# Performance work log

Measured on AMD Instinct MI355X. Metric: run time of the kernel, lower is better.

The kernel has to match this reference:

```python
import jax, jax.numpy as jnp
import numpy as np

# ---- module configuration (from init_kwargs) ----
NX, NV = 2048, 1024
LX = 1.0
VMAX = 6.0
DX = LX / NX
DV = 2.0 * VMAX / NV
XS = jnp.linspace(-LX / 2 + DX / 2, LX / 2 - DX / 2, NX)
VS = jnp.linspace(-VMAX + DV / 2, VMAX - DV / 2, NV)
AE, AI = 1.0, 1836.0
ZE, ZI = -1.0, 1.0
OMEGA_C_TAU = 1.0
NU_EE, NU_II = 1.0, 0.1
DT = 1e-3
T_LBO = 1.0  # LBO temperature, u = 0


def minmod(a, b):
    return jnp.where(a * b > 0, jnp.sign(a) * jnp.minimum(jnp.abs(a), jnp.abs(b)), 0.0)


def _sl(a, lo, hi, axis):
    return jax.lax.slice_in_dim(a, lo, hi, axis=axis)


def slope_limited_flux_divergence(f_pad, F, dx, axis):
    # f_pad has N+4 cells along `axis` (2 ghost cells per side). MUSCL + minmod.
    n = f_pad.shape[axis]
    d = _sl(f_pad, 1, n, axis) - _sl(f_pad, 0, n - 1, axis)          # n-1 diffs
    sigma = minmod(_sl(d, 0, n - 2, axis), _sl(d, 1, n - 1, axis))    # slopes for cells 1..n-2
    fc = _sl(f_pad, 1, n - 1, axis)                                   # cells 1..n-2
    m = n - 2
    fL = _sl(fc, 0, m - 1, axis) + 0.5 * _sl(sigma, 0, m - 1, axis)   # left interface states
    fR = _sl(fc, 1, m, axis) - 0.5 * _sl(sigma, 1, m, axis)           # right interface states
    flux = F(fL, fR)                                                  # N+1 interface fluxes
    k = flux.shape[axis]
    return (_sl(flux, 1, k, axis) - _sl(flux, 0, k - 1, axis)) / dx   # N cells


def pad_x_periodic(f):
    return jnp.concatenate([f[-2:, :], f, f[:2, :]], axis=0)


def pad_v_zero(f):
    z = jnp.zeros((f.shape[0], 2), f.dtype)
    return jnp.concatenate([z, f, z], axis=1)


def poisson_solve(rho_c):
    # dE/dx = rho_c, zero-mean E (periodic-compatible gauge)
    E = jnp.cumsum(rho_c) * DX
    return E - jnp.mean(E)


def species_rhs(f, E, A, Z):
    v = VS[None, :]
    Fx = lambda l, r: jnp.where(v > 0, l * v, r * v)                  # upwind in x
    vdfdx = slope_limited_flux_divergence(pad_x_periodic(f), Fx, DX, axis=0)
    Ec = (OMEGA_C_TAU * Z / A) * E[:, None]
    Fv = lambda l, r: jnp.where(Ec > 0, l * Ec, r * Ec)               # upwind in v
    Edfdv = slope_limited_flux_divergence(pad_v_zero(f), Fv, DV, axis=1)
    return -vdfdx - Edfdv


def vlasov_rhs(fe, fi):
    ne = jnp.sum(fe, axis=1) * DV
    ni = jnp.sum(fi, axis=1) * DV
    E = poisson_solve(ZE * ne + ZI * ni)
    return species_rhs(fe, E, AE, ZE), species_rhs(fi, E, AI, ZI)


def ssprk2(fe, fi, dt):
    re, ri = vlasov_rhs(fe, fi)
    fe1, fi1 = fe + dt * re, fi + dt * ri
    re1, ri1 = vlasov_rhs(fe1, fi1)
    return 0.5 * (fe + fe1 + dt * re1), 0.5 * (fi + fi1 + dt * ri1)


def lbo_diagonals(lam):
    # L f = lam * d/dv( v f + T df/dv ), central differences
    vm = jnp.roll(VS, 1)
    vp = jnp.roll(VS, -1)
    dl = lam * (T_LBO / DV**2 - vm / (2 * DV))
    du = lam * (T_LBO / DV**2 + vp / (2 * DV))
    d = lam * (-2.0 * T_LBO / DV**2) * jnp.ones(NV, XS.dtype)
    return dl.at[0].set(0.0), d, du.at[-1].set(0.0)


def nu_shape():
    midpt = LX / 3
    ef = LX / 6 / 10
    h0 = lambda x: 1 + jnp.exp(x / ef - midpt / ef)
    return 1.0 / (0.5 * (h0(XS) + h0(-XS)))  # [Nx]


def thomas(dl, d, du, b):
    # Thomas algorithm; dl[0]==0 and du[-1]==0 assumed.
    def fwd(carry, inp):
        cp, bp = carry
        dli, di, dui, bi = inp
        m = di - dli * cp
        cpi = dui / m
        bpi = (bi - dli * bp) / m
        return (cpi, bpi), (cpi, bpi)
    z = jnp.zeros((), b.dtype)
    _, (cp, bp) = jax.lax.scan(fwd, (z, z), (dl, d, du, b))
    def bwd(x_next, inp):
        cpi, bpi = inp
        x = bpi - cpi * x_next
        return x, x
    _, x = jax.lax.scan(bwd, z, (cp, bp), reverse=True)
    return x


def implicit_collide(f, lam, dt):
    dl, d, du = lbo_diagonals(lam)
    nu = nu_shape()
    def solve_row(nui, frow):
        return thomas(-dt * nui * dl, 1.0 - dt * nui * d, -dt * nui * du, frow)
    return jax.vmap(solve_row)(nu, f)


def setup_inputs() -> dict:
    key = jax.random.key(0)
    k1, k2 = jax.random.split(key)
    fe = jax.random.uniform(k1, (NX, NV), dtype=jnp.float32)
    fi = jax.random.uniform(k2, (NX, NV), dtype=jnp.float32)
    return {"fe": fe, "fi": fi}


def reference(fe, fi):
    fe1, fi1 = ssprk2(fe, fi, DT)
    fe2 = implicit_collide(fe1, NU_EE, DT)
    fi2 = implicit_collide(fi1, NU_II, DT)
    return jnp.stack([fe2, fi2])  # [2, Nx, Nv]
```

## Files before the change

kernel.cpp:

```cpp
#include <hip/hip_runtime.h>
#include <math.h>

#define NX 2048
#define NV 1024

static constexpr float DXf    = 1.0f / 2048.0f;
static constexpr float DVf    = 12.0f / 1024.0f;
static constexpr float DTf    = 0.001f;
static constexpr float INV_DX = 2048.0f;
static constexpr float INV_DV = 1024.0f / 12.0f;

__device__ __forceinline__ float minmod_f(float a, float b) {
    return (a * b > 0.0f) ? (a > 0.0f ? fminf(a, b) : fmaxf(a, b)) : 0.0f;
}

__device__ __forceinline__ float frcp(float x) {
    float r = __builtin_amdgcn_rcpf(x);
    return r * (2.0f - x * r);
}

__device__ __forceinline__ int swz2048(int x) {
    return ((x & 7) << 8) + (x >> 3);
}

__device__ __forceinline__ void rhs4(const float* __restrict__ g, int i, int j0, float Ec,
                                     float4& f0v, float4& rv) {
    const float* rowc = g + i * NV;
    const float* rm1  = g + (((i - 1) & (NX - 1)) * NV);
    const float* rm2  = g + (((i - 2) & (NX - 1)) * NV);
    const float* rp1  = g + (((i + 1) & (NX - 1)) * NV);
    const float* rp2  = g + (((i + 2) & (NX - 1)) * NV);

    float4 c   = *(const float4*)(rowc + j0);
    float4 xm1 = *(const float4*)(rm1 + j0);
    float4 xm2 = *(const float4*)(rm2 + j0);
    float4 xp1 = *(const float4*)(rp1 + j0);
    float4 xp2 = *(const float4*)(rp2 + j0);
    float4 lm = make_float4(0.f, 0.f, 0.f, 0.f);
    float4 rp = make_float4(0.f, 0.f, 0.f, 0.f);
    if (j0 >= 4)      lm = *(const float4*)(rowc + j0 - 4);
    if (j0 <= NV - 8) rp = *(const float4*)(rowc + j0 + 4);

    float vals[8] = {lm.z, lm.w, c.x, c.y, c.z, c.w, rp.x, rp.y};
    const float* cc   = (const float*)&c;
    const float* am1  = (const float*)&xm1;
    const float* am2  = (const float*)&xm2;
    const float* ap1  = (const float*)&xp1;
    const float* ap2  = (const float*)&xp2;
    float* f0o = (float*)&f0v;
    float* ro  = (float*)&rv;

    #pragma unroll
    for (int k = 0; k < 4; ++k) {
        float f0  = cc[k];
        float fm1 = am1[k], fm2 = am2[k], fp1 = ap1[k], fp2 = ap2[k];

        float v = DVf * ((float)(j0 + k) + 0.5f) - 6.0f;
        float dm1 = fm1 - fm2, d0 = f0 - fm1, dp1 = fp1 - f0, dp2 = fp2 - fp1;
        float sm1 = minmod_f(dm1, d0);
        float s0  = minmod_f(d0, dp1);
        float sp1 = minmod_f(dp1, dp2);
        float PhiM, PhiP;
        if (v > 0.0f) {
            PhiM = (fm1 + 0.5f * sm1) * v;
            PhiP = (f0  + 0.5f * s0 ) * v;
        } else {
            PhiM = (f0  - 0.5f * s0 ) * v;
            PhiP = (fp1 - 0.5f * sp1) * v;
        }
        float vdfdx = (PhiP - PhiM) * INV_DX;

        float gm2 = vals[k], gm1 = vals[k + 1], gp1 = vals[k + 3], gp2 = vals[k + 4];
        float em1 = gm1 - gm2, e0 = f0 - gm1, ep1 = gp1 - f0, ep2 = gp2 - gp1;
        float tm1 = minmod_f(em1, e0);
        float t0  = minmod_f(e0, ep1);
        float tp1 = minmod_f(ep1, ep2);
        float GM, GP;
        if (Ec > 0.0f) {
            GM = (gm1 + 0.5f * tm1) * Ec;
            GP = (f0  + 0.5f * t0 ) * Ec;
        } else {
            GM = (f0  - 0.5f * t0 ) * Ec;
            GP = (gp1 - 0.5f * tp1) * Ec;
        }
        float Edfdv = (GP - GM) * INV_DV;

        f0o[k] = f0;
        ro[k]  = -vdfdx - Edfdv;
    }
}

__global__ __launch_bounds__(256) void moments_kernel(const float* __restrict__ fe,
                                                      const float* __restrict__ fi,
                                                      float* __restrict__ se,
                                                      float* __restrict__ si) {
    const int row = swz2048(blockIdx.x);
    const int t = threadIdx.x, lane = t & 63, wv = t >> 6;
    float4 x = *(const float4*)(fe + (size_t)row * NV + 4 * t);
    float4 y = *(const float4*)(fi + (size_t)row * NV + 4 * t);
    float a = x.x + x.y + x.z + x.w;
    float b = y.x + y.y + y.z + y.w;
    #pragma unroll
    for (int off = 32; off > 0; off >>= 1) {
        a += __shfl_down(a, off, 64);
        b += __shfl_down(b, off, 64);
    }
    __shared__ float r1[4], r2[4];
    if (lane == 0) { r1[wv] = a; r2[wv] = b; }
    __syncthreads();
    if (t == 0) {
        se[row] = r1[0] + r1[1] + r1[2] + r1[3];
        si[row] = r2[0] + r2[1] + r2[2] + r2[3];
    }
}

__global__ __launch_bounds__(256) void escan_kernel(const float* __restrict__ se_,
                                                    const float* __restrict__ si_,
                                                    float* __restrict__ E) {
    const int t = threadIdx.x, lane = t & 63, wv = t >> 6;
    const int k0 = t * 8;
    float4 a0 = *(const float4*)(se_ + k0);
    float4 a1 = *(const float4*)(se_ + k0 + 4);
    float4 b0 = *(const float4*)(si_ + k0);
    float4 b1 = *(const float4*)(si_ + k0 + 4);
    float rho[8];
    rho[0] = DVf * (b0.x - a0.x); rho[1] = DVf * (b0.y - a0.y);
    rho[2] = DVf * (b0.z - a0.z); rho[3] = DVf * (b0.w - a0.w);
    rho[4] = DVf * (b1.x - a1.x); rho[5] = DVf * (b1.y - a1.y);
    rho[6] = DVf * (b1.z - a1.z); rho[7] = DVf * (b1.w - a1.w);
    float s = 0.0f, w = 0.0f;
    #pragma unroll
    for (int r = 0; r < 8; ++r) {
        s += rho[r];
        w += rho[r] * (float)(NX - (k0 + r));
    }
    float sc = s;
    #pragma unroll
    for (int off = 1; off < 64; off <<= 1) {
        float u = __shfl_up(sc, off, 64);
        if (lane >= off) sc += u;
    }
    #pragma unroll
    for (int off = 32; off > 0; off >>= 1) w += __shfl_down(w, off, 64);
    __shared__ float wsum[4], wtot[4];
    if (lane == 63) wsum[wv] = sc;
    if (lane == 0)  wtot[wv] = w;
    __syncthreads();
    float base = 0.0f;
    #pragma unroll
    for (int u = 0; u < 4; ++u) if (u < wv) base += wsum[u];
    float W = wtot[0] + wtot[1] + wtot[2] + wtot[3];
    float run = base + sc - s;
    const float mean = W * (1.0f / (float)NX);
    #pragma unroll
    for (int r = 0; r < 8; ++r) {
        run += rho[r];
        E[k0 + r] = DXf * (run - mean);
    }
}

__global__ __launch_bounds__(256) void stage1_kernel(const float* __restrict__ fe,
                                                     const float* __restrict__ fi,
                                                     const float* __restrict__ E0,
                                                     float* __restrict__ fe1,
                                                     float* __restrict__ fi1,
                                                     float* __restrict__ se1,
                                                     float* __restrict__ si1) {
    const int row = swz2048(blockIdx.x);
    const int sp  = blockIdx.y;
    const float* f = sp ? fi : fe;
    float* f1 = sp ? fi1 : fe1;
    const float zoa = sp ? (1.0f / 1836.0f) : -1.0f;
    const float Ec = zoa * E0[row];
    const int t = threadIdx.x, lane = t & 63, wv = t >> 6;
    const int j0 = 4 * t;

    float4 f0v, rv;
    rhs4(f, row, j0, Ec, f0v, rv);
    float4 o;
    o.x = f0v.x + DTf * rv.x;
    o.y = f0v.y + DTf * rv.y;
    o.z = f0v.z + DTf * rv.z;
    o.w = f0v.w + DTf * rv.w;
    *(float4*)(f1 + (size_t)row * NV + j0) = o;

    float s = o.x + o.y + o.z + o.w;
    #pragma unroll
    for (int off = 32; off > 0; off >>= 1) s += __shfl_down(s, off, 64);
    __shared__ float sred[4];
    if (lane == 0) sred[wv] = s;
    __syncthreads();
    if (t == 0) (sp ? si1 : se1)[row] = sred[0] + sred[1] + sred[2] + sred[3];
}

__global__ __launch_bounds__(64) void stage2_collide_kernel(
    const float* __restrict__ fe, const float* __restrict__ fi,
    const float* __restrict__ fe1, const float* __restrict__ fi1,
    const float* __restrict__ E1,
    float* __restrict__ out) {
    const int row = swz2048(blockIdx.x);
    const int sp  = blockIdx.y;
    const int lane = threadIdx.x & 63;
    const float* h  = sp ? fi : fe;
    const float* f1 = sp ? fi1 : fe1;
    const float zoa = sp ? (1.0f / 1836.0f) : -1.0f;
    const float lam = sp ? 0.1f : 1.0f;
    const float Ec = zoa * E1[row];
    float* orow = out + ((size_t)sp * NX + row) * NV;

    const float Tdv2   = 1.0f / (DVf * DVf);
    const float inv2dv = 0.5f / DVf;
    const float xi = DXf * ((float)row + 0.5f) - 0.5f;
    const float nu = 1.0f / (1.0f + 0.5f * (expf(60.0f * xi - 20.0f) + expf(-60.0f * xi - 20.0f)));
    const float K = DTf * nu * lam;
    const float b = 1.0f + 2.0f * K * Tdv2;

    const int j0 = 16 * lane;

    float Dv[16], Av[16], Cv[16];
    #pragma unroll
    for (int q = 0; q < 4; ++q) {
        float4 f0v, rv;
        rhs4(f1, row, j0 + 4 * q, Ec, f0v, rv);
        float4 h4 = *(const float4*)(h + (size_t)row * NV + j0 + 4 * q);
        float dq[4];
        dq[0] = 0.5f * h4.x + 0.5f * f0v.x + (0.5f * DTf) * rv.x;
        dq[1] = 0.5f * h4.y + 0.5f * f0v.y + (0.5f * DTf) * rv.y;
        dq[2] = 0.5f * h4.z + 0.5f * f0v.z + (0.5f * DTf) * rv.z;
        dq[3] = 0.5f * h4.w + 0.5f * f0v.w + (0.5f * DTf) * rv.w;
        #pragma unroll
        for (int rr = 0; rr < 4; ++rr) {
            const int r = 4 * q + rr;
            const int j = j0 + r;
            float a = (j == 0)      ? 0.0f : -K * (Tdv2 - (DVf * ((float)j - 0.5f) - 6.0f) * inv2dv);
            float c = (j == NV - 1) ? 0.0f : -K * (Tdv2 + (DVf * ((float)j + 1.5f) - 6.0f) * inv2dv);
            if (r == 0) {
                float e = frcp(b);
                Dv[0] = e * dq[0];
                Av[0] = e * a;
                Cv[0] = e * c;
            } else {
                float e = frcp(b - a * Cv[r - 1]);
                Dv[r] = e * (dq[rr] - a * Dv[r - 1]);
                Av[r] = -e * a * Av[r - 1];
                Cv[r] = e * c;
            }
        }
    }
    #pragma unroll
    for (int r = 14; r >= 0; --r) {
        Dv[r] = Dv[r] - Cv[r] * Dv[r + 1];
        Av[r] = Av[r] - Cv[r] * Av[r + 1];
        Cv[r] = -Cv[r] * Cv[r + 1];
    }

    float la = Av[0],  ra = Cv[0],  d0 = Dv[0];
    float lb = Av[15], rb = Cv[15], d1 = Dv[15];
    #pragma unroll
    for (int s = 1; s < 64; s <<= 1) {
        float lb_m = __shfl_up(lb, s, 64);
        float rb_m = __shfl_up(rb, s, 64);
        float d1_m = __shfl_up(d1, s, 64);
        if (lane < s) { lb_m = 0.0f; rb_m = 0.0f; d1_m = 0.0f; }
        float la_p = __shfl_down(la, s, 64);
        float ra_p = __shfl_down(ra, s, 64);
        float d0_p = __shfl_down(d0, s, 64);
        if (lane + s > 63) { la_p = 0.0f; ra_p = 0.0f; d0_p = 0.0f; }

        float m00 = 1.0f - la * rb_m;
        float m01 = -ra * la_p;
        float m10 = -lb * rb_m;
        float m11 = 1.0f - rb * la_p;
        float idet = frcp(m00 * m11 - m01 * m10);

        float Lr0 = -la * lb_m, Lr1 = -lb * lb_m;
        float Rr0 = -ra * ra_p, Rr1 = -rb * ra_p;
        float e0 = d0 - la * d1_m - ra * d0_p;
        float e1 = d1 - lb * d1_m - rb * d0_p;

        la = idet * (m11 * Lr0 - m01 * Lr1);
        lb = idet * (m00 * Lr1 - m10 * Lr0);
        ra = idet * (m11 * Rr0 - m01 * Rr1);
        rb = idet * (m00 * Rr1 - m10 * Rr0);
        d0 = idet * (m11 * e0 - m01 * e1);
        d1 = idet * (m00 * e1 - m10 * e0);
    }
    float zl = __shfl_up(d1, 1, 64);
    if (lane == 0) zl = 0.0f;
    float yr = __shfl_down(d0, 1, 64);
    if (lane == 63) yr = 0.0f;

    #pragma unroll
    for (int r = 0; r < 16; ++r) Dv[r] = Dv[r] - Av[r] * zl - Cv[r] * yr;
    #pragma unroll
    for (int q = 0; q < 4; ++q) {
        float4 o;
        o.x = Dv[4 * q + 0];
        o.y = Dv[4 * q + 1];
        o.z = Dv[4 * q + 2];
        o.w = Dv[4 * q + 3];
        *(float4*)(orow + j0 + 4 * q) = o;
    }
}

extern "C" void kernel_launch(void* const* d_in, const int* in_sizes, int n_in,
                              void* d_out, int out_size, void* d_ws, size_t ws_size,
                              hipStream_t stream) {
    const float* fe = (const float*)d_in[0];
    const float* fi = (const float*)d_in[1];
    float* out = (float*)d_out;
    const size_t P = (size_t)NX * NV;

    float* fe1 = (float*)d_ws;
    float* fi1 = fe1 + P;
    float* se  = fi1 + P;
    float* si  = se + NX;
    float* se1 = si + NX;
    float* si1 = se1 + NX;
    float* E0  = si1 + NX;
    float* E1  = E0 + NX;

    dim3 rgrid(2048, 2);

    moments_kernel<<<2048, 256, 0, stream>>>(fe, fi, se, si);
    escan_kernel<<<1, 256, 0, stream>>>(se, si, E0);
    stage1_kernel<<<rgrid, 256, 0, stream>>>(fe, fi, E0, fe1, fi1, se1, si1);
    escan_kernel<<<1, 256, 0, stream>>>(se1, si1, E1);
    stage2_collide_kernel<<<rgrid, 64, 0, stream>>>(fe, fi, fe1, fi1, E1, out);
}
```

Baseline: 115.3 us.

## Split stage-2 RHS from tridiagonal collide into separate kernels; drop Newton refinement in rcp

Unfuses the second SSP-RK stage RHS computation from the implicit collision solve. The RHS now runs in a 256-thread-per-row kernel writing into the output buffer, and a 64-thread collide kernel reads that buffer back and solves in place. The aim is better parallelism for the stencil work, which was previously done by only 64 threads per row. The cost is an extra full-array write and read plus one more launch. The reciprocal also drops its Newton refinement step, which trades accuracy for fewer instructions.

```diff
diff --git a/kernel.cpp b/kernel.cpp
--- a/kernel.cpp
+++ b/kernel.cpp
@@ -15,8 +15,7 @@
 }
 
 __device__ __forceinline__ float frcp(float x) {
-    float r = __builtin_amdgcn_rcpf(x);
-    return r * (2.0f - x * r);
+    return __builtin_amdgcn_rcpf(x);
 }
 
 __device__ __forceinline__ int swz2048(int x) {
@@ -193,19 +192,38 @@
     if (t == 0) (sp ? si1 : se1)[row] = sred[0] + sred[1] + sred[2] + sred[3];
 }
 
-__global__ __launch_bounds__(64) void stage2_collide_kernel(
-    const float* __restrict__ fe, const float* __restrict__ fi,
-    const float* __restrict__ fe1, const float* __restrict__ fi1,
-    const float* __restrict__ E1,
-    float* __restrict__ out) {
+__global__ __launch_bounds__(256) void stage2_rhs_kernel(const float* __restrict__ fe,
+                                                         const float* __restrict__ fi,
+                                                         const float* __restrict__ fe1,
+                                                         const float* __restrict__ fi1,
+                                                         const float* __restrict__ E1,
+                                                         float* __restrict__ out) {
+    const int row = swz2048(blockIdx.x);
+    const int sp  = blockIdx.y;
+    const float* h  = sp ? fi : fe;
+    const float* f1 = sp ? fi1 : fe1;
+    const float zoa = sp ? (1.0f / 1836.0f) : -1.0f;
+    const float Ec = zoa * E1[row];
+    const int t = threadIdx.x;
+    const int j0 = 4 * t;
+    float* orow = out + ((size_t)sp * NX + row) * NV;
+
+    float4 f0v, rv;
+    rhs4(f1, row, j0, Ec, f0v, rv);
+    float4 h4 = *(const float4*)(h + (size_t)row * NV + j0);
+    float4 o;
+    o.x = 0.5f * h4.x + 0.5f * f0v.x + (0.5f * DTf) * rv.x;
+    o.y = 0.5f * h4.y + 0.5f * f0v.y + (0.5f * DTf) * rv.y;
+    o.z = 0.5f * h4.z + 0.5f * f0v.z + (0.5f * DTf) * rv.z;
+    o.w = 0.5f * h4.w + 0.5f * f0v.w + (0.5f * DTf) * rv.w;
+    *(float4*)(orow + j0) = o;
+}
+
+__global__ __launch_bounds__(64) void collide_kernel(float* __restrict__ out) {
     const int row = swz2048(blockIdx.x);
     const int sp  = blockIdx.y;
     const int lane = threadIdx.x & 63;
-    const float* h  = sp ? fi : fe;
-    const float* f1 = sp ? fi1 : fe1;
-    const float zoa = sp ? (1.0f / 1836.0f) : -1.0f;
     const float lam = sp ? 0.1f : 1.0f;
-    const float Ec = zoa * E1[row];
     float* orow = out + ((size_t)sp * NX + row) * NV;
 
     const float Tdv2   = 1.0f / (DVf * DVf);
@@ -217,34 +235,29 @@
 
     const int j0 = 16 * lane;
 
+    float4 q0 = *(const float4*)(orow + j0);
+    float4 q1 = *(const float4*)(orow + j0 + 4);
+    float4 q2 = *(const float4*)(orow + j0 + 8);
+    float4 q3 = *(const float4*)(orow + j0 + 12);
+    float d[16] = {q0.x, q0.y, q0.z, q0.w, q1.x, q1.y, q1.z, q1.w,
+                   q2.x, q2.y, q2.z, q2.w, q3.x, q3.y, q3.z, q3.w};
+
     float Dv[16], Av[16], Cv[16];
     #pragma unroll
-    for (int q = 0; q < 4; ++q) {
-        float4 f0v, rv;
-        rhs4(f1, row, j0 + 4 * q, Ec, f0v, rv);
-        float4 h4 = *(const float4*)(h + (size_t)row * NV + j0 + 4 * q);
-        float dq[4];
-        dq[0] = 0.5f * h4.x + 0.5f * f0v.x + (0.5f * DTf) * rv.x;
-        dq[1] = 0.5f * h4.y + 0.5f * f0v.y + (0.5f * DTf) * rv.y;
-        dq[2] = 0.5f * h4.z + 0.5f * f0v.z + (0.5f * DTf) * rv.z;
-        dq[3] = 0.5f * h4.w + 0.5f * f0v.w + (0.5f * DTf) * rv.w;
-        #pragma unroll
-        for (int rr = 0; rr < 4; ++rr) {
-            const int r = 4 * q + rr;
-            const int j = j0 + r;
-            float a = (j == 0)      ? 0.0f : -K * (Tdv2 - (DVf * ((float)j - 0.5f) - 6.0f) * inv2dv);
-            float c = (j == NV - 1) ? 0.0f : -K * (Tdv2 + (DVf * ((float)j + 1.5f) - 6.0f) * inv2dv);
-            if (r == 0) {
-                float e = frcp(b);
-                Dv[0] = e * dq[0];
-                Av[0] = e * a;
-                Cv[0] = e * c;
-            } else {
-                float e = frcp(b - a * Cv[r - 1]);
-                Dv[r] = e * (dq[rr] - a * Dv[r - 1]);
-                Av[r] = -e * a * Av[r - 1];
-                Cv[r] = e * c;
-            }
+    for (int r = 0; r < 16; ++r) {
+        const int j = j0 + r;
+        float a = (j == 0)      ? 0.0f : -K * (Tdv2 - (DVf * ((float)j - 0.5f) - 6.0f) * inv2dv);
+        float c = (j == NV - 1) ? 0.0f : -K * (Tdv2 + (DVf * ((float)j + 1.5f) - 6.0f) * inv2dv);
+        if (r == 0) {
+            float e = frcp(b);
+            Dv[0] = e * d[0];
+            Av[0] = e * a;
+            Cv[0] = e * c;
+        } else {
+            float e = frcp(b - a * Cv[r - 1]);
+            Dv[r] = e * (d[r] - a * Dv[r - 1]);
+            Av[r] = -e * a * Av[r - 1];
+            Cv[r] = e * c;
         }
     }
     #pragma unroll
@@ -326,5 +339,6 @@
     escan_kernel<<<1, 256, 0, stream>>>(se, si, E0);
     stage1_kernel<<<rgrid, 256, 0, stream>>>(fe, fi, E0, fe1, fi1, se1, si1);
     escan_kernel<<<1, 256, 0, stream>>>(se1, si1, E1);
-    stage2_collide_kernel<<<rgrid, 64, 0, stream>>>(fe, fi, fe1, fi1, E1, out);
-}
+    stage2_rhs_kernel<<<rgrid, 256, 0, stream>>>(fe, fi, fe1, fi1, E1, out);
+    collide_kernel<<<rgrid, 64, 0, stream>>>(out);
+}
```

Result: faster. 111.8 us (-3.0%).
